# Kernel optimization log

Measured on AMD Instinct MI355X. Metric: run time of the kernel, lower is better.

Reference implementation:

```python
import jax, jax.numpy as jnp
import numpy as np

B, S, D = 2, 2048, 1024
H = 16
KEY_DIM = 1024   # full projected dim; original scales by sqrt(key_dim), NOT head_dim
VAL_DIM = 1024
OUT_DIM = 1024


def setup_inputs() -> dict:
    key = jax.random.key(0)
    ks = jax.random.split(key, 11)
    s = 0.02
    return {
        "queries": jax.random.normal(ks[0], (B, S, D), jnp.float32),
        "keys": jax.random.normal(ks[1], (B, S, D), jnp.float32),
        "values": jax.random.normal(ks[2], (B, S, D), jnp.float32),
        "Wq": jax.random.normal(ks[3], (D, KEY_DIM), jnp.float32) * s,
        "bq": jnp.zeros((KEY_DIM,), jnp.float32),
        "Wk": jax.random.normal(ks[4], (D, KEY_DIM), jnp.float32) * s,
        "bk": jnp.zeros((KEY_DIM,), jnp.float32),
        "Wv": jax.random.normal(ks[5], (D, VAL_DIM), jnp.float32) * s,
        "bv": jnp.zeros((VAL_DIM,), jnp.float32),
        "Wo": jax.random.normal(ks[6], (KEY_DIM, OUT_DIM), jnp.float32) * s,
        "bo": jnp.zeros((OUT_DIM,), jnp.float32),
    }


def _split_heads(x):
    # [B, S, H*dh] -> [B, H, S, dh]
    b, s, _ = x.shape
    return x.reshape(b, s, H, -1).transpose(0, 2, 1, 3)


def reference(queries, keys, values, Wq, bq, Wk, bk, Wv, bv, Wo, bo):
    q = _split_heads(queries @ Wq + bq)   # [B,H,S,dk]
    k = _split_heads(keys @ Wk + bk)      # [B,H,S,dk]
    v = _split_heads(values @ Wv + bv)    # [B,H,S,dv]
    scale = jnp.sqrt(jnp.float32(KEY_DIM))  # full key_dim, as in the source
    scores = jnp.einsum('bhqd,bhkd->bhqk', q, k) / scale  # [B,H,S,S]
    # Source calls F.softmax with no dim; torch's legacy rule picks dim=1
    # (the heads axis) for a 4-D tensor. Reproduced faithfully.
    weights = jax.nn.softmax(scores, axis=1)
    o = jnp.einsum('bhqk,bhkd->bhqd', weights, v)          # [B,H,S,dv]
    o = o.transpose(0, 2, 1, 3).reshape(B, S, KEY_DIM)     # merge heads
    return o @ Wo + bo
```

## Files before the change

### kernel.cpp

```cpp
#include <hip/hip_runtime.h>


typedef unsigned short ushort;
typedef __attribute__((ext_vector_type(8))) short short8;
typedef __attribute__((ext_vector_type(4))) short short4v;
typedef __attribute__((ext_vector_type(4))) float f32x4;
typedef __attribute__((ext_vector_type(4))) float float4v;
typedef __attribute__((ext_vector_type(4))) unsigned int uint4v;
typedef __attribute__((ext_vector_type(2))) unsigned int uint2v;

#define MFMA32(a, b, c) __builtin_amdgcn_mfma_f32_16x16x32_bf16(a, b, c, 0, 0, 0)
#define MFMA16(a, b, c) __builtin_amdgcn_mfma_f32_16x16x16bf16_1k(a, b, c, 0, 0, 0)

__device__ __forceinline__ ushort f2bf(float f) {
    unsigned u = __float_as_uint(f);
    u += 0x7fffu + ((u >> 16) & 1u);
    return (ushort)(u >> 16);
}
__device__ __forceinline__ float bf2f(ushort u) {
    return __uint_as_float(((unsigned)u) << 16);
}

__device__ __forceinline__ void gload16(const ushort* g, ushort* l) {
    __builtin_amdgcn_global_load_lds(
        (__attribute__((address_space(1))) void*)(unsigned long long)(g),
        (__attribute__((address_space(3))) void*)(l), 16, 0, 0);
}

__global__ __launch_bounds__(256) void convert_x_kernel(
    const float* __restrict__ q, const float* __restrict__ k,
    const float* __restrict__ v, ushort* __restrict__ out) {
    const size_t NPER = 4194304ull;
    size_t idx = ((size_t)blockIdx.x * 256 + threadIdx.x) * 8;
    const size_t stride = (size_t)gridDim.x * 256 * 8;
    for (; idx < 3 * NPER; idx += stride) {
        const float* src;
        size_t off;
        if (idx < NPER)          { src = q; off = idx; }
        else if (idx < 2 * NPER) { src = k; off = idx - NPER; }
        else                     { src = v; off = idx - 2 * NPER; }
        float4v a = *(const float4v*)(src + off);
        float4v b = *(const float4v*)(src + off + 4);
        union { ushort u[8]; uint4v v4; } pk;
        #pragma unroll
        for (int j = 0; j < 4; j++) { pk.u[j] = f2bf(a[j]); pk.u[4 + j] = f2bf(b[j]); }
        *(uint4v*)(out + idx) = pk.v4;
    }
}

__global__ __launch_bounds__(256) void transpose_w_kernel(
    const float* __restrict__ w0, const float* __restrict__ w1,
    const float* __restrict__ w2, const float* __restrict__ w3,
    ushort* __restrict__ Wt) {
    const float* W = blockIdx.z == 0 ? w0 : blockIdx.z == 1 ? w1 : blockIdx.z == 2 ? w2 : w3;
    ushort* out = Wt + (size_t)blockIdx.z * 1024 * 1024;
    __shared__ ushort st[64 * 72];
    int t = threadIdx.x;
    int kb = blockIdx.y * 64, nb = blockIdx.x * 64;
    int c4 = (t & 15) * 4;
    int r0 = t >> 4;
    #pragma unroll
    for (int p = 0; p < 4; p++) {
        int r = r0 + p * 16;
        float4v f = *(const float4v*)(W + (size_t)(kb + r) * 1024 + nb + c4);
        union { ushort u[4]; uint2v v2; } pk;
        #pragma unroll
        for (int j = 0; j < 4; j++) pk.u[j] = f2bf(f[j]);
        *(uint2v*)(st + r * 72 + c4) = pk.v2;
    }
    __syncthreads();
    int n = t >> 2;
    int kc = (t & 3) * 16;
    union { ushort u[16]; uint4v v4[2]; } tw;
    #pragma unroll
    for (int j = 0; j < 16; j++) tw.u[j] = st[(kc + j) * 72 + n];
    uint4v* dst = (uint4v*)(out + (size_t)(nb + n) * 1024 + kb + kc);
    dst[0] = tw.v4[0];
    dst[1] = tw.v4[1];
}

__device__ __forceinline__ void gemm_core(
    const ushort* __restrict__ A, const ushort* __restrict__ Bt,
    const float* __restrict__ bias, ushort* __restrict__ Cb,
    float* __restrict__ Cf, int mode, ushort* sA, ushort* sB) {
    int tid = threadIdx.x, lane = tid & 63, wave = tid >> 6;
    int li = lane & 15, g = lane >> 4;
    int mt = blockIdx.y * 128, nt = blockIdx.x * 128;
    int wm = (wave >> 1) * 64, wn = (wave & 1) * 64;
    f32x4 acc[4][4] = {};
    for (int k0 = 0; k0 < 1024; k0 += 64) {
        __syncthreads();
        #pragma unroll
        for (int i = 0; i < 4; i++) {
            int c = tid + i * 256;
            int row = c >> 3, chd = c & 7;
            int cg = chd ^ (row & 7);
            gload16(A + (size_t)(mt + row) * 1024 + k0 + cg * 8, sA + c * 8);
            gload16(Bt + (size_t)(nt + row) * 1024 + k0 + cg * 8, sB + c * 8);
        }
        __syncthreads();
        #pragma unroll
        for (int kk = 0; kk < 2; kk++) {
            short8 af[4], bfr[4];
            #pragma unroll
            for (int i = 0; i < 4; i++) {
                int ra = wm + i * 16 + li;
                int cb = kk * 64 + g * 16;
                af[i] = *(const short8*)((char*)sA + ra * 128 + (cb ^ ((ra & 7) << 4)));
                int rb = wn + i * 16 + li;
                bfr[i] = *(const short8*)((char*)sB + rb * 128 + (cb ^ ((rb & 7) << 4)));
            }
            #pragma unroll
            for (int mi = 0; mi < 4; mi++)
                #pragma unroll
                for (int ni = 0; ni < 4; ni++)
                    acc[mi][ni] = MFMA32(af[mi], bfr[ni], acc[mi][ni]);
        }
    }
    #pragma unroll
    for (int mi = 0; mi < 4; mi++) {
        #pragma unroll
        for (int ni = 0; ni < 4; ni++) {
            int n = nt + wn + ni * 16 + li;
            int m0 = mt + wm + mi * 16 + g * 4;
            float bv = bias[n];
            if (mode == 0) {
                #pragma unroll
                for (int r = 0; r < 4; r++)
                    Cb[(size_t)(m0 + r) * 1024 + n] = f2bf(acc[mi][ni][r] + bv);
            } else if (mode == 1) {
                int batch = m0 >> 11, mm = m0 & 2047;
                union { ushort u[4]; uint2v v2; } pk;
                #pragma unroll
                for (int r = 0; r < 4; r++) pk.u[r] = f2bf(acc[mi][ni][r] + bv);
                *(uint2v*)(Cb + (size_t)batch * 1024 * 2048 + (size_t)n * 2048 + mm) = pk.v2;
            } else {
                #pragma unroll
                for (int r = 0; r < 4; r++)
                    Cf[(size_t)(m0 + r) * 1024 + n] = acc[mi][ni][r] + bv;
            }
        }
    }
}

__global__ __launch_bounds__(256, 2) void proj_kernel(
    const ushort* __restrict__ Xb, const ushort* __restrict__ Wt,
    const float* __restrict__ bq, const float* __restrict__ bk,
    const float* __restrict__ bv, ushort* __restrict__ Qb,
    ushort* __restrict__ Kb, ushort* __restrict__ Vtb) {
    __shared__ ushort sA[128 * 64];
    __shared__ ushort sB[128 * 64];
    int z = blockIdx.z;
    const float* bias = z == 0 ? bq : (z == 1 ? bk : bv);
    ushort* out = z == 0 ? Qb : (z == 1 ? Kb : Vtb);
    gemm_core(Xb + (size_t)z * 4194304ull, Wt + (size_t)z * 1048576ull,
              bias, out, nullptr, z == 2 ? 1 : 0, sA, sB);
}

__global__ __launch_bounds__(256, 2) void outproj_kernel(
    const ushort* __restrict__ Ob, const ushort* __restrict__ Wt3,
    const float* __restrict__ bo, float* __restrict__ out) {
    __shared__ ushort sA[128 * 64];
    __shared__ ushort sB[128 * 64];
    gemm_core(Ob, Wt3, bo, nullptr, out, 2, sA, sB);
}

__global__ __launch_bounds__(256, 2) void zsum_kernel(
    const ushort* __restrict__ Qb, const ushort* __restrict__ Kb,
    ushort* __restrict__ Zinv) {
    __shared__ ushort sQ[64 * 64];
    __shared__ ushort sK[128 * 64];
    int tid = threadIdx.x, lane = tid & 63, wid = tid >> 6;
    int li = lane & 15, g = lane >> 4;
    int bid = blockIdx.x;
    int swz = (bid & 7) * 128 + (bid >> 3);
    int qt = swz & 31, C = swz >> 5;
    int b = C >> 4, kg = C & 15;
    int q0 = qt * 64, k0 = kg * 128;
    const ushort* Qp = Qb + (size_t)(b * 2048 + q0) * 1024;
    const ushort* Kp = Kb + (size_t)(b * 2048 + k0) * 1024;
    f32x4 zacc[4][2] = {};
    for (int h = 0; h < 16; h++) {
        int co = h * 64;
        __syncthreads();
        #pragma unroll
        for (int i = 0; i < 2; i++) {
            int c = tid + i * 256;
            int r = c >> 3, m = c & 7;
            gload16(Qp + (size_t)r * 1024 + co + (m ^ (r & 7)) * 8, sQ + c * 8);
        }
        #pragma unroll
        for (int i = 0; i < 4; i++) {
            int c = tid + i * 256;
            int r = c >> 3, m = c & 7;
            gload16(Kp + (size_t)r * 1024 + co + (m ^ (r & 7)) * 8, sK + c * 8);
        }
        __syncthreads();
        short8 qf[4][2], kf[2][2];
        #pragma unroll
        for (int qs = 0; qs < 4; qs++)
            #pragma unroll
            for (int dc = 0; dc < 2; dc++) {
                int row = qs * 16 + li;
                qf[qs][dc] = *(const short8*)(
                    (char*)sQ + row * 128 + ((dc * 64 + g * 16) ^ ((row & 7) << 4)));
            }
        #pragma unroll
        for (int ks = 0; ks < 2; ks++)
            #pragma unroll
            for (int dc = 0; dc < 2; dc++) {
                int row = wid * 32 + ks * 16 + li;
                kf[ks][dc] = *(const short8*)(
                    (char*)sK + row * 128 + ((dc * 64 + g * 16) ^ ((row & 7) << 4)));
            }
        #pragma unroll
        for (int qs = 0; qs < 4; qs++)
            #pragma unroll
            for (int ks = 0; ks < 2; ks++) {
                f32x4 st = {0.f, 0.f, 0.f, 0.f};
                st = MFMA32(kf[ks][0], qf[qs][0], st);
                st = MFMA32(kf[ks][1], qf[qs][1], st);
                #pragma unroll
                for (int r = 0; r < 4; r++)
                    zacc[qs][ks][r] += __expf(st[r] * 0.03125f);
            }
    }
    #pragma unroll
    for (int qs = 0; qs < 4; qs++)
        #pragma unroll
        for (int ks = 0; ks < 2; ks++) {
            union { ushort u[4]; uint2v v; } pk;
            #pragma unroll
            for (int r = 0; r < 4; r++)
                pk.u[r] = f2bf(__builtin_amdgcn_rcpf(zacc[qs][ks][r]));
            *(uint2v*)(Zinv + (size_t)(b * 2048 + q0 + qs * 16 + li) * 2048 +
                       k0 + wid * 32 + ks * 16 + g * 4) = pk.v;
        }
}

__global__ __launch_bounds__(256, 2) void pv_kernel(
    const ushort* __restrict__ Qb, const ushort* __restrict__ Kb,
    const ushort* __restrict__ Vt, const ushort* __restrict__ Zinv,
    ushort* __restrict__ Ob) {
    __shared__ ushort sK[2][4 * 32 * 64];
    __shared__ ushort sV[2][4 * 64 * 32];
    __shared__ ushort sZ[2][32 * 32];
    int tid = threadIdx.x, lane = tid & 63, hh = tid >> 6;
    int li = lane & 15, g = lane >> 4;
    int bid = blockIdx.x;
    int swz = (bid & 7) * 64 + (bid >> 3);
    int hp = swz & 3, p = swz >> 2;
    int b = p >> 6, qt = p & 63;
    int q0 = qt * 32;
    int head = hp * 4 + hh;
    short8 qf[2][2];
    #pragma unroll
    for (int qs = 0; qs < 2; qs++)
        #pragma unroll
        for (int dc = 0; dc < 2; dc++)
            qf[qs][dc] = *(const short8*)(
                Qb + (size_t)(b * 2048 + q0 + qs * 16 + li) * 1024 +
                head * 64 + dc * 32 + g * 8);
    f32x4 oacc[2][4] = {};
    int kc_h = 0, kc_r = (tid >> 3) & 31, kc_m = tid & 7;
    int vc_r = (tid >> 2) & 63, vc_m = tid & 3;
    int zc_r = tid >> 2, zc_m = tid & 3;
    const ushort* Kst = Kb + (size_t)(b * 2048 + kc_r) * 1024 + hp * 256 +
                        (kc_m ^ (kc_r & 7)) * 8;
    const ushort* Vst = Vt + (size_t)(b * 1024 + hp * 256 + vc_r) * 2048 +
                        (vc_m ^ ((vc_r >> 1) & 3)) * 8;
    const ushort* Zst = Zinv + (size_t)(b * 2048 + q0 + zc_r) * 2048 +
                        (zc_m ^ ((zc_r >> 1) & 3)) * 8;
    #define PV_STAGE(BUF, KB)                                                  \
        {                                                                      \
            _Pragma("unroll") for (int i = 0; i < 4; i++)                      \
                gload16(Kst + (size_t)(KB) * 1024 + i * 64,                    \
                        sK[BUF] + (tid + i * 256) * 8);                        \
            _Pragma("unroll") for (int i = 0; i < 4; i++)                      \
                gload16(Vst + (size_t)i * 64 * 2048 + (KB),                    \
                        sV[BUF] + (tid + i * 256) * 8);                        \
            if (tid < 128) gload16(Zst + (KB), sZ[BUF] + tid * 8);             \
        }
    PV_STAGE(0, 0)
    __syncthreads();
    for (int it = 0; it < 64; ++it) {
        int cur = it & 1;
        int kb = it * 32;
        if (it + 1 < 64) PV_STAGE(cur ^ 1, kb + 32)
        short8 kf[2][2];
        #pragma unroll
        for (int ks = 0; ks < 2; ks++)
            #pragma unroll
            for (int dc = 0; dc < 2; dc++) {
                int rk = ks * 16 + li;
                kf[ks][dc] = *(const short8*)(
                    (char*)sK[cur] + hh * 4096 + rk * 128 +
                    ((dc * 64 + g * 16) ^ ((rk & 7) << 4)));
            }
        short4v pf[2][2];
        #pragma unroll
        for (int qs = 0; qs < 2; qs++)
            #pragma unroll
            for (int ks = 0; ks < 2; ks++) {
                f32x4 st = {0.f, 0.f, 0.f, 0.f};
                st = MFMA32(kf[ks][0], qf[qs][0], st);
                st = MFMA32(kf[ks][1], qf[qs][1], st);
                int sl = ks * 4 + g;
                int rq = qs * 16 + li;
                union { ushort u[4]; uint2v v; } rz;
                rz.v = *(const uint2v*)(
                    (char*)sZ[cur] + rq * 64 +
                    (((sl >> 1) ^ ((li >> 1) & 3)) * 2 + (sl & 1)) * 8);
                short4v pp;
                #pragma unroll
                for (int r = 0; r < 4; r++)
                    pp[r] = (short)f2bf(__expf(st[r] * 0.03125f) * bf2f(rz.u[r]));
                pf[qs][ks] = pp;
            }
        #pragma unroll
        for (int ks = 0; ks < 2; ks++) {
            int sl = ks * 4 + g;
            #pragma unroll
            for (int ds = 0; ds < 4; ds++) {
                int rv = ds * 16 + li;
                short4v vf = *(const short4v*)(
                    (char*)sV[cur] + hh * 4096 + rv * 64 +
                    (((sl >> 1) ^ ((li >> 1) & 3)) * 2 + (sl & 1)) * 8);
                oacc[0][ds] = MFMA16(pf[0][ks], vf, oacc[0][ds]);
                oacc[1][ds] = MFMA16(pf[1][ks], vf, oacc[1][ds]);
            }
        }
        __syncthreads();
    }
    #undef PV_STAGE
    ushort* Oo = Ob + (size_t)(b * 2048 + q0) * 1024 + head * 64;
    #pragma unroll
    for (int qs = 0; qs < 2; qs++)
        #pragma unroll
        for (int ds = 0; ds < 4; ds++)
            #pragma unroll
            for (int r = 0; r < 4; r++)
                Oo[(size_t)(qs * 16 + g * 4 + r) * 1024 + ds * 16 + li] =
                    f2bf(oacc[qs][ds][r]);
}

extern "C" void kernel_launch(void* const* d_in, const int* in_sizes, int n_in,
                              void* d_out, int out_size, void* d_ws, size_t ws_size,
                              hipStream_t stream) {
    const float* queries = (const float*)d_in[0];
    const float* keys    = (const float*)d_in[1];
    const float* values  = (const float*)d_in[2];
    const float* Wq = (const float*)d_in[3];
    const float* bq = (const float*)d_in[4];
    const float* Wk = (const float*)d_in[5];
    const float* bk = (const float*)d_in[6];
    const float* Wv = (const float*)d_in[7];
    const float* bv = (const float*)d_in[8];
    const float* Wo = (const float*)d_in[9];
    const float* bo = (const float*)d_in[10];
    float* out = (float*)d_out;

    ushort* Xb  = (ushort*)d_ws;
    ushort* Wt  = Xb + 12ull * 1024 * 1024;
    ushort* Qb  = Wt + 4ull * 1024 * 1024;
    ushort* Kb  = Qb + 4ull * 1024 * 1024;
    ushort* Vtb = Kb + 4ull * 1024 * 1024;
    ushort* Zinv = Xb;
    ushort* Ob   = Xb + 8ull * 1024 * 1024;

    convert_x_kernel<<<2048, 256, 0, stream>>>(queries, keys, values, Xb);
    transpose_w_kernel<<<dim3(16, 16, 4), 256, 0, stream>>>(Wq, Wk, Wv, Wo, Wt);
    proj_kernel<<<dim3(8, 32, 3), 256, 0, stream>>>(Xb, Wt, bq, bk, bv, Qb, Kb, Vtb);
    zsum_kernel<<<1024, 256, 0, stream>>>(Qb, Kb, Zinv);
    pv_kernel<<<512, 256, 0, stream>>>(Qb, Kb, Vtb, Zinv, Ob);
    outproj_kernel<<<dim3(8, 32), 256, 0, stream>>>(Ob, Wt + 3ull * 1024 * 1024, bo, out);
}
```

Before: 194.9 us.

## Store log-sum in fp16 and double query rows per pv block for K/V reuse

New measurement: 230.0 us. +18.0%, slower.

```diff
diff --git a/kernel.cpp b/kernel.cpp
--- a/kernel.cpp
+++ b/kernel.cpp
@@ -12,13 +12,22 @@
 #define MFMA32(a, b, c) __builtin_amdgcn_mfma_f32_16x16x32_bf16(a, b, c, 0, 0, 0)
 #define MFMA16(a, b, c) __builtin_amdgcn_mfma_f32_16x16x16bf16_1k(a, b, c, 0, 0, 0)
 
+#define C2SCALE 0.045084220027780106f
+
 __device__ __forceinline__ ushort f2bf(float f) {
     unsigned u = __float_as_uint(f);
     u += 0x7fffu + ((u >> 16) & 1u);
     return (ushort)(u >> 16);
 }
-__device__ __forceinline__ float bf2f(ushort u) {
-    return __uint_as_float(((unsigned)u) << 16);
+__device__ __forceinline__ ushort f2hf(float f) {
+    union { _Float16 h; ushort u; } c;
+    c.h = (_Float16)f;
+    return c.u;
+}
+__device__ __forceinline__ float hf2f(ushort h) {
+    union { ushort u; _Float16 h; } c;
+    c.u = h;
+    return (float)c.h;
 }
 
 __device__ __forceinline__ void gload16(const ushort* g, ushort* l) {
@@ -222,7 +231,7 @@
                 st = MFMA32(kf[ks][1], qf[qs][1], st);
                 #pragma unroll
                 for (int r = 0; r < 4; r++)
-                    zacc[qs][ks][r] += __expf(st[r] * 0.03125f);
+                    zacc[qs][ks][r] += exp2f(st[r] * C2SCALE);
             }
     }
     #pragma unroll
@@ -232,26 +241,25 @@
             union { ushort u[4]; uint2v v; } pk;
             #pragma unroll
             for (int r = 0; r < 4; r++)
-                pk.u[r] = f2bf(__builtin_amdgcn_rcpf(zacc[qs][ks][r]));
+                pk.u[r] = f2hf(__log2f(zacc[qs][ks][r]));
             *(uint2v*)(Zinv + (size_t)(b * 2048 + q0 + qs * 16 + li) * 2048 +
                        k0 + wid * 32 + ks * 16 + g * 4) = pk.v;
         }
 }
 
-__global__ __launch_bounds__(256, 2) void pv_kernel(
+__global__ __launch_bounds__(512, 2) void pv_kernel(
     const ushort* __restrict__ Qb, const ushort* __restrict__ Kb,
     const ushort* __restrict__ Vt, const ushort* __restrict__ Zinv,
     ushort* __restrict__ Ob) {
     __shared__ ushort sK[2][4 * 32 * 64];
     __shared__ ushort sV[2][4 * 64 * 32];
-    __shared__ ushort sZ[2][32 * 32];
-    int tid = threadIdx.x, lane = tid & 63, hh = tid >> 6;
+    __shared__ ushort sZ[2][64 * 32];
+    int tid = threadIdx.x, lane = tid & 63, wave = tid >> 6;
     int li = lane & 15, g = lane >> 4;
     int bid = blockIdx.x;
-    int swz = (bid & 7) * 64 + (bid >> 3);
-    int hp = swz & 3, p = swz >> 2;
-    int b = p >> 6, qt = p & 63;
-    int q0 = qt * 32;
+    int hp = bid & 3, b = (bid >> 2) & 1, qt = bid >> 3;
+    int q0 = qt * 64;
+    int hh = wave & 3, qg = wave >> 2;
     int head = hp * 4 + hh;
     short8 qf[2][2];
     #pragma unroll
@@ -259,27 +267,28 @@
         #pragma unroll
         for (int dc = 0; dc < 2; dc++)
             qf[qs][dc] = *(const short8*)(
-                Qb + (size_t)(b * 2048 + q0 + qs * 16 + li) * 1024 +
+                Qb + (size_t)(b * 2048 + q0 + qg * 32 + qs * 16 + li) * 1024 +
                 head * 64 + dc * 32 + g * 8);
     f32x4 oacc[2][4] = {};
-    int kc_h = 0, kc_r = (tid >> 3) & 31, kc_m = tid & 7;
+    int kc_r = (tid >> 3) & 31, kc_m = tid & 7;
     int vc_r = (tid >> 2) & 63, vc_m = tid & 3;
     int zc_r = tid >> 2, zc_m = tid & 3;
+    int th2 = tid >> 8;
     const ushort* Kst = Kb + (size_t)(b * 2048 + kc_r) * 1024 + hp * 256 +
-                        (kc_m ^ (kc_r & 7)) * 8;
-    const ushort* Vst = Vt + (size_t)(b * 1024 + hp * 256 + vc_r) * 2048 +
+                        th2 * 64 + (kc_m ^ (kc_r & 7)) * 8;
+    const ushort* Vst = Vt + (size_t)(b * 1024 + hp * 256 + th2 * 64 + vc_r) * 2048 +
                         (vc_m ^ ((vc_r >> 1) & 3)) * 8;
     const ushort* Zst = Zinv + (size_t)(b * 2048 + q0 + zc_r) * 2048 +
                         (zc_m ^ ((zc_r >> 1) & 3)) * 8;
     #define PV_STAGE(BUF, KB)                                                  \
         {                                                                      \
-            _Pragma("unroll") for (int i = 0; i < 4; i++)                      \
-                gload16(Kst + (size_t)(KB) * 1024 + i * 64,                    \
-                        sK[BUF] + (tid + i * 256) * 8);                        \
-            _Pragma("unroll") for (int i = 0; i < 4; i++)                      \
-                gload16(Vst + (size_t)i * 64 * 2048 + (KB),                    \
-                        sV[BUF] + (tid + i * 256) * 8);                        \
-            if (tid < 128) gload16(Zst + (KB), sZ[BUF] + tid * 8);             \
+            _Pragma("unroll") for (int i = 0; i < 2; i++)                      \
+                gload16(Kst + (size_t)(KB) * 1024 + i * 128,                   \
+                        sK[BUF] + (tid + i * 512) * 8);                        \
+            _Pragma("unroll") for (int i = 0; i < 2; i++)                      \
+                gload16(Vst + (size_t)i * 128 * 2048 + (KB),                   \
+                        sV[BUF] + (tid + i * 512) * 8);                        \
+            if (tid < 256) gload16(Zst + (KB), sZ[BUF] + tid * 8);             \
         }
     PV_STAGE(0, 0)
     __syncthreads();
@@ -306,15 +315,17 @@
                 st = MFMA32(kf[ks][0], qf[qs][0], st);
                 st = MFMA32(kf[ks][1], qf[qs][1], st);
                 int sl = ks * 4 + g;
-                int rq = qs * 16 + li;
+                int rq = qg * 32 + qs * 16 + li;
                 union { ushort u[4]; uint2v v; } rz;
                 rz.v = *(const uint2v*)(
                     (char*)sZ[cur] + rq * 64 +
-                    (((sl >> 1) ^ ((li >> 1) & 3)) * 2 + (sl & 1)) * 8);
+                    (((sl >> 1) ^ ((rq >> 1) & 3)) * 2 + (sl & 1)) * 8);
                 short4v pp;
                 #pragma unroll
-                for (int r = 0; r < 4; r++)
-                    pp[r] = (short)f2bf(__expf(st[r] * 0.03125f) * bf2f(rz.u[r]));
+                for (int r = 0; r < 4; r++) {
+                    float e = exp2f(__builtin_fmaf(st[r], C2SCALE, -hf2f(rz.u[r])));
+                    pp[r] = (short)f2bf(e);
+                }
                 pf[qs][ks] = pp;
             }
         #pragma unroll
@@ -325,7 +336,7 @@
                 int rv = ds * 16 + li;
                 short4v vf = *(const short4v*)(
                     (char*)sV[cur] + hh * 4096 + rv * 64 +
-                    (((sl >> 1) ^ ((li >> 1) & 3)) * 2 + (sl & 1)) * 8);
+                    (((sl >> 1) ^ ((rv >> 1) & 3)) * 2 + (sl & 1)) * 8);
                 oacc[0][ds] = MFMA16(pf[0][ks], vf, oacc[0][ds]);
                 oacc[1][ds] = MFMA16(pf[1][ks], vf, oacc[1][ds]);
             }
@@ -333,7 +344,7 @@
         __syncthreads();
     }
     #undef PV_STAGE
-    ushort* Oo = Ob + (size_t)(b * 2048 + q0) * 1024 + head * 64;
+    ushort* Oo = Ob + (size_t)(b * 2048 + q0 + qg * 32) * 1024 + head * 64;
     #pragma unroll
     for (int qs = 0; qs < 2; qs++)
         #pragma unroll
@@ -372,6 +383,6 @@
     transpose_w_kernel<<<dim3(16, 16, 4), 256, 0, stream>>>(Wq, Wk, Wv, Wo, Wt);
     proj_kernel<<<dim3(8, 32, 3), 256, 0, stream>>>(Xb, Wt, bq, bk, bv, Qb, Kb, Vtb);
     zsum_kernel<<<1024, 256, 0, stream>>>(Qb, Kb, Zinv);
-    pv_kernel<<<512, 256, 0, stream>>>(Qb, Kb, Vtb, Zinv, Ob);
+    pv_kernel<<<256, 512, 0, stream>>>(Qb, Kb, Vtb, Zinv, Ob);
     outproj_kernel<<<dim3(8, 32), 256, 0, stream>>>(Ob, Wt + 3ull * 1024 * 1024, bo, out);
 }
```

## Store log-normalizer and use fine-grained vmcnt waits in PV loop

Applied to the files above, without the earlier changes.

New measurement: 188.1 us. 1.04x faster.

```diff
diff --git a/kernel.cpp b/kernel.cpp
--- a/kernel.cpp
+++ b/kernel.cpp
@@ -12,13 +12,24 @@
 #define MFMA32(a, b, c) __builtin_amdgcn_mfma_f32_16x16x32_bf16(a, b, c, 0, 0, 0)
 #define MFMA16(a, b, c) __builtin_amdgcn_mfma_f32_16x16x16bf16_1k(a, b, c, 0, 0, 0)
 
+#define VMCNT(N) asm volatile("s_waitcnt vmcnt(" #N ")" ::: "memory")
+#define SCHEDBAR() __builtin_amdgcn_sched_barrier(0)
+#define BARRIER() __builtin_amdgcn_s_barrier()
+
 __device__ __forceinline__ ushort f2bf(float f) {
     unsigned u = __float_as_uint(f);
     u += 0x7fffu + ((u >> 16) & 1u);
     return (ushort)(u >> 16);
 }
-__device__ __forceinline__ float bf2f(ushort u) {
-    return __uint_as_float(((unsigned)u) << 16);
+__device__ __forceinline__ ushort f2hf(float f) {
+    union { _Float16 h; ushort u; } c;
+    c.h = (_Float16)f;
+    return c.u;
+}
+__device__ __forceinline__ float hf2f(ushort h) {
+    union { ushort u; _Float16 h; } c;
+    c.u = h;
+    return (float)c.h;
 }
 
 __device__ __forceinline__ void gload16(const ushort* g, ushort* l) {
@@ -167,7 +178,7 @@
 
 __global__ __launch_bounds__(256, 2) void zsum_kernel(
     const ushort* __restrict__ Qb, const ushort* __restrict__ Kb,
-    ushort* __restrict__ Zinv) {
+    ushort* __restrict__ Zln) {
     __shared__ ushort sQ[64 * 64];
     __shared__ ushort sK[128 * 64];
     int tid = threadIdx.x, lane = tid & 63, wid = tid >> 6;
@@ -232,15 +243,15 @@
             union { ushort u[4]; uint2v v; } pk;
             #pragma unroll
             for (int r = 0; r < 4; r++)
-                pk.u[r] = f2bf(__builtin_amdgcn_rcpf(zacc[qs][ks][r]));
-            *(uint2v*)(Zinv + (size_t)(b * 2048 + q0 + qs * 16 + li) * 2048 +
+                pk.u[r] = f2hf(__logf(zacc[qs][ks][r]));
+            *(uint2v*)(Zln + (size_t)(b * 2048 + q0 + qs * 16 + li) * 2048 +
                        k0 + wid * 32 + ks * 16 + g * 4) = pk.v;
         }
 }
 
 __global__ __launch_bounds__(256, 2) void pv_kernel(
     const ushort* __restrict__ Qb, const ushort* __restrict__ Kb,
-    const ushort* __restrict__ Vt, const ushort* __restrict__ Zinv,
+    const ushort* __restrict__ Vt, const ushort* __restrict__ Zln,
     ushort* __restrict__ Ob) {
     __shared__ ushort sK[2][4 * 32 * 64];
     __shared__ ushort sV[2][4 * 64 * 32];
@@ -262,14 +273,14 @@
                 Qb + (size_t)(b * 2048 + q0 + qs * 16 + li) * 1024 +
                 head * 64 + dc * 32 + g * 8);
     f32x4 oacc[2][4] = {};
-    int kc_h = 0, kc_r = (tid >> 3) & 31, kc_m = tid & 7;
+    int kc_r = (tid >> 3) & 31, kc_m = tid & 7;
     int vc_r = (tid >> 2) & 63, vc_m = tid & 3;
-    int zc_r = tid >> 2, zc_m = tid & 3;
+    int zc_r = (tid & 127) >> 2, zc_m = tid & 3;
     const ushort* Kst = Kb + (size_t)(b * 2048 + kc_r) * 1024 + hp * 256 +
                         (kc_m ^ (kc_r & 7)) * 8;
     const ushort* Vst = Vt + (size_t)(b * 1024 + hp * 256 + vc_r) * 2048 +
                         (vc_m ^ ((vc_r >> 1) & 3)) * 8;
-    const ushort* Zst = Zinv + (size_t)(b * 2048 + q0 + zc_r) * 2048 +
+    const ushort* Zst = Zln + (size_t)(b * 2048 + q0 + zc_r) * 2048 +
                         (zc_m ^ ((zc_r >> 1) & 3)) * 8;
     #define PV_STAGE(BUF, KB)                                                  \
         {                                                                      \
@@ -282,11 +293,17 @@
             if (tid < 128) gload16(Zst + (KB), sZ[BUF] + tid * 8);             \
         }
     PV_STAGE(0, 0)
-    __syncthreads();
     for (int it = 0; it < 64; ++it) {
         int cur = it & 1;
         int kb = it * 32;
-        if (it + 1 < 64) PV_STAGE(cur ^ 1, kb + 32)
+        if (it + 1 < 64) {
+            PV_STAGE(cur ^ 1, kb + 32)
+            if (hh < 2) { VMCNT(9); } else { VMCNT(8); }
+        } else {
+            VMCNT(0);
+        }
+        SCHEDBAR();
+        BARRIER();
         short8 kf[2][2];
         #pragma unroll
         for (int ks = 0; ks < 2; ks++)
@@ -310,12 +327,19 @@
                 union { ushort u[4]; uint2v v; } rz;
                 rz.v = *(const uint2v*)(
                     (char*)sZ[cur] + rq * 64 +
-                    (((sl >> 1) ^ ((li >> 1) & 3)) * 2 + (sl & 1)) * 8);
-                short4v pp;
-                #pragma unroll
-                for (int r = 0; r < 4; r++)
-                    pp[r] = (short)f2bf(__expf(st[r] * 0.03125f) * bf2f(rz.u[r]));
-                pf[qs][ks] = pp;
+                    (((sl >> 1) ^ ((rq >> 1) & 3)) * 2 + (sl & 1)) * 8);
+                float e0 = __expf(__builtin_fmaf(st[0], 0.03125f, -hf2f(rz.u[0])));
+                float e1 = __expf(__builtin_fmaf(st[1], 0.03125f, -hf2f(rz.u[1])));
+                float e2 = __expf(__builtin_fmaf(st[2], 0.03125f, -hf2f(rz.u[2])));
+                float e3 = __expf(__builtin_fmaf(st[3], 0.03125f, -hf2f(rz.u[3])));
+                unsigned a0 = __float_as_uint(e0) + 0x8000u;
+                unsigned a1 = __float_as_uint(e1) + 0x8000u;
+                unsigned a2 = __float_as_uint(e2) + 0x8000u;
+                unsigned a3 = __float_as_uint(e3) + 0x8000u;
+                union { unsigned u[2]; short4v s; } pk;
+                pk.u[0] = __builtin_amdgcn_perm(a1, a0, 0x07060302u);
+                pk.u[1] = __builtin_amdgcn_perm(a3, a2, 0x07060302u);
+                pf[qs][ks] = pk.s;
             }
         #pragma unroll
         for (int ks = 0; ks < 2; ks++) {
@@ -325,12 +349,12 @@
                 int rv = ds * 16 + li;
                 short4v vf = *(const short4v*)(
                     (char*)sV[cur] + hh * 4096 + rv * 64 +
-                    (((sl >> 1) ^ ((li >> 1) & 3)) * 2 + (sl & 1)) * 8);
+                    (((sl >> 1) ^ ((rv >> 1) & 3)) * 2 + (sl & 1)) * 8);
                 oacc[0][ds] = MFMA16(pf[0][ks], vf, oacc[0][ds]);
                 oacc[1][ds] = MFMA16(pf[1][ks], vf, oacc[1][ds]);
             }
         }
-        __syncthreads();
+        BARRIER();
     }
     #undef PV_STAGE
     ushort* Oo = Ob + (size_t)(b * 2048 + q0) * 1024 + head * 64;
@@ -365,13 +389,13 @@
     ushort* Qb  = Wt + 4ull * 1024 * 1024;
     ushort* Kb  = Qb + 4ull * 1024 * 1024;
     ushort* Vtb = Kb + 4ull * 1024 * 1024;
-    ushort* Zinv = Xb;
-    ushort* Ob   = Xb + 8ull * 1024 * 1024;
+    ushort* Zln = Xb;
+    ushort* Ob  = Xb + 8ull * 1024 * 1024;
 
     convert_x_kernel<<<2048, 256, 0, stream>>>(queries, keys, values, Xb);
     transpose_w_kernel<<<dim3(16, 16, 4), 256, 0, stream>>>(Wq, Wk, Wv, Wo, Wt);
     proj_kernel<<<dim3(8, 32, 3), 256, 0, stream>>>(Xb, Wt, bq, bk, bv, Qb, Kb, Vtb);
-    zsum_kernel<<<1024, 256, 0, stream>>>(Qb, Kb, Zinv);
-    pv_kernel<<<512, 256, 0, stream>>>(Qb, Kb, Vtb, Zinv, Ob);
+    zsum_kernel<<<1024, 256, 0, stream>>>(Qb, Kb, Zln);
+    pv_kernel<<<512, 256, 0, stream>>>(Qb, Kb, Vtb, Zln, Ob);
     outproj_kernel<<<dim3(8, 32), 256, 0, stream>>>(Ob, Wt + 3ull * 1024 * 1024, bo, out);
 }
```
